# Kernel tuning notes

Hardware: AMD Instinct MI355X
Metric: run time of the kernel (lower is better)

## Reference

```python
import jax, jax.numpy as jnp
import numpy as np

B, C, T, K = 16, 256, 2048, 1024

def setup_inputs() -> dict:
    key = jax.random.key(0)
    k1, k2 = jax.random.split(key)
    z = jax.random.normal(k1, (B, C, T), dtype=jnp.float32)
    codebook = jax.random.normal(k2, (K, C), dtype=jnp.float32)
    return {"z": z, "codebook": codebook}

def reference(z, codebook):
    # z: (B, C, T) -> z_flat: (B*T, C)
    Bsz, Ch, Tlen = z.shape
    z_flat = jnp.transpose(z, (0, 2, 1)).reshape(-1, Ch)
    # squared L2 distances: |z|^2 - 2 z.c + |c|^2  -> (B*T, K)
    distances = (
        jnp.sum(z_flat * z_flat, axis=1, keepdims=True)
        - 2.0 * (z_flat @ codebook.T)
        + jnp.sum(codebook * codebook, axis=1)[None, :]
    )
    indices = jnp.argmin(distances, axis=1)            # (B*T,)
    z_q_flat = codebook[indices]                       # (B*T, C)
    z_q = jnp.transpose(z_q_flat.reshape(Bsz, Tlen, Ch), (0, 2, 1))  # (B, C, T)
    indices_reshaped = indices.reshape(Bsz, Tlen)      # (B, T)
    return z_q, indices_reshaped
```

## Files before the change

### kernel.cpp

```cpp
#include <hip/hip_runtime.h>

#define NB 16
#define NC 256
#define NT 2048
#define NK 1024
#define TQB 128
#define NCHUNKS 32
#define HALF_B 16384
#define CHUNK_B 32768
#define AMB_TH 0.05f

typedef __attribute__((ext_vector_type(8))) short short8v;
typedef __attribute__((ext_vector_type(16))) float f32x16;

__device__ __forceinline__ unsigned bf16_rne(float x) {
  unsigned u = __float_as_uint(x);
  return (u + 0x7FFFu + ((u >> 16) & 1u)) >> 16;
}

__global__ __launch_bounds__(256) void vq_prep(const float* __restrict__ cb,
                                               char* __restrict__ cbs,
                                               float* __restrict__ cnorm) {
  const int k = blockIdx.x, c = threadIdx.x;
  float v = cb[k * NC + c];
  unsigned hb = bf16_rne(v);
  float hf = __uint_as_float(hb << 16);
  unsigned lb = bf16_rne(v - hf);
  const int chunk = k >> 5, r = k & 31;
  const int off = (r << 9) + (((((c >> 3)) ^ r) & 31) << 4) + ((c & 7) << 1);
  *(unsigned short*)(cbs + (size_t)chunk * CHUNK_B + off) = (unsigned short)hb;
  *(unsigned short*)(cbs + (size_t)chunk * CHUNK_B + HALF_B + off) = (unsigned short)lb;
  float s = v * v;
  #pragma unroll
  for (int o = 32; o > 0; o >>= 1) s += __shfl_down(s, o, 64);
  __shared__ float wsum[4];
  if ((threadIdx.x & 63) == 0) wsum[threadIdx.x >> 6] = s;
  __syncthreads();
  if (threadIdx.x == 0) cnorm[k] = 0.5f * (wsum[0] + wsum[1] + wsum[2] + wsum[3]);
}

__global__ __launch_bounds__(256, 1) void vq_main(const float* __restrict__ z,
                                                  const char* __restrict__ cbs,
                                                  const float* __restrict__ cnorm,
                                                  const float* __restrict__ cb,
                                                  float* __restrict__ out,
                                                  int* __restrict__ flags) {
  __shared__ char ldsb[2 * CHUNK_B];
  __shared__ int idx_sh[TQB];
  __shared__ int amb_sh[TQB];
  const int tid = threadIdx.x;
  const int w = tid >> 6, l = tid & 63;
  const int r = l & 31;
  const int h = l >> 5;
  const int b = blockIdx.x >> 4;
  const int t0 = (blockIdx.x & 15) * TQB;
  const int tq = t0 + (w << 5) + r;

  short8v Ahi[16], Alo[16];
  #pragma unroll
  for (int s = 0; s < 16; ++s) {
    const float* zp = z + ((size_t)(b * NC + (s << 4) + (h << 3))) * NT + tq;
    #pragma unroll
    for (int e = 0; e < 8; ++e) {
      float v = zp[(size_t)e * NT];
      unsigned hb = bf16_rne(v);
      float hf = __uint_as_float(hb << 16);
      unsigned lb = bf16_rne(v - hf);
      Ahi[s][e] = (short)hb;
      Alo[s][e] = (short)lb;
    }
  }

  float bestv[16], secv[16];
  int besti[16];
  #pragma unroll
  for (int i = 0; i < 16; ++i) {
    bestv[i] = -3.402823466e38f; secv[i] = -3.402823466e38f; besti[i] = 0;
  }

#define STAGE(CH, BSEL) do {                                                      \
    const char* _s = cbs + (size_t)(CH) * CHUNK_B + ((size_t)tid << 4);           \
    char* _d = ldsb + (BSEL) * CHUNK_B + (w << 10);                               \
    _Pragma("unroll")                                                             \
    for (int _j = 0; _j < 8; ++_j)                                                \
      __builtin_amdgcn_global_load_lds(                                           \
          (const __attribute__((address_space(1))) void*)(_s + (_j << 12)),       \
          (__attribute__((address_space(3))) void*)(_d + (_j << 12)), 16, 0, 0);  \
  } while (0)

  STAGE(0, 0);
  int bufsel = 0;
  for (int ch = 0; ch < NCHUNKS; ++ch) {
    STAGE((ch + 1) & (NCHUNKS - 1), bufsel ^ 1);
    asm volatile("s_waitcnt vmcnt(8)" ::: "memory");
    __builtin_amdgcn_s_barrier();
    float cn = cnorm[(ch << 5) + r];
    f32x16 accA = {}, accB = {}, accC = {};
    const char* Lh = ldsb + bufsel * CHUNK_B;
    #pragma unroll
    for (int s = 0; s < 16; ++s) {
      const int off = (r << 9) + (((((s << 1) + h) ^ r) & 31) << 4);
      short8v Bh = *(const short8v*)(Lh + off);
      short8v Bl = *(const short8v*)(Lh + HALF_B + off);
      accA = __builtin_amdgcn_mfma_f32_32x32x16_bf16(Ahi[s], Bh, accA, 0, 0, 0);
      accB = __builtin_amdgcn_mfma_f32_32x32x16_bf16(Ahi[s], Bl, accB, 0, 0, 0);
      accC = __builtin_amdgcn_mfma_f32_32x32x16_bf16(Alo[s], Bh, accC, 0, 0, 0);
    }
    __builtin_amdgcn_s_barrier();
    const int kidx = (ch << 5) + r;
    #pragma unroll
    for (int i = 0; i < 16; ++i) {
      float sc = (accA[i] + accB[i] + accC[i]) - cn;
      if (sc > bestv[i]) { secv[i] = bestv[i]; bestv[i] = sc; besti[i] = kidx; }
      else               { secv[i] = fmaxf(secv[i], sc); }
    }
    bufsel ^= 1;
  }
#undef STAGE

  #pragma unroll
  for (int st = 1; st < 32; st <<= 1) {
    #pragma unroll
    for (int i = 0; i < 16; ++i) {
      float ob = __shfl_xor(bestv[i], st, 64);
      float os = __shfl_xor(secv[i], st, 64);
      int   oi = __shfl_xor(besti[i], st, 64);
      if (ob > bestv[i]) {
        secv[i] = fmaxf(bestv[i], os);
        bestv[i] = ob; besti[i] = oi;
      } else {
        secv[i] = fmaxf(secv[i], ob);
        if (ob == bestv[i] && oi < besti[i]) besti[i] = oi;
      }
    }
  }
  if (r == 0) {
    #pragma unroll
    for (int i = 0; i < 16; ++i) {
      const int row = (i & 3) + ((i >> 2) << 3) + (h << 2);
      idx_sh[(w << 5) + row] = besti[i];
      amb_sh[(w << 5) + row] = (bestv[i] - secv[i] <= AMB_TH) ? 1 : 0;
    }
  }
  asm volatile("s_waitcnt vmcnt(0)" ::: "memory");
  __syncthreads();

  if (tid < TQB) {
    const int t = t0 + tid;
    out[(size_t)NB * NC * NT + (size_t)b * NT + t] = (float)idx_sh[tid];
    flags[b * NT + t] = amb_sh[tid];
  }

  const int tt = tid & 127;
  const int chi = tid >> 7;
  const int myidx = idx_sh[tt];
  const float* crow = cb + (size_t)myidx * NC;
  const size_t obase = (size_t)b * NC * NT + (size_t)t0 + tt;
  #pragma unroll 8
  for (int c0 = 0; c0 < NC; c0 += 2) {
    const int c = c0 + chi;
    out[obase + (size_t)c * NT] = crow[c];
  }
}

__global__ __launch_bounds__(256) void vq_cleanup(const float* __restrict__ z,
                                                  const float* __restrict__ cb,
                                                  const int* __restrict__ flags,
                                                  float* __restrict__ out) {
  const int q = blockIdx.x;
  if (!flags[q]) return;
  const int b = q >> 11, t = q & (NT - 1);
  __shared__ float zsh[NC];
  __shared__ unsigned long long red[5];
  const int tid = threadIdx.x;
  zsh[tid] = z[((size_t)b * NC + tid) * NT + t];
  __syncthreads();
  float bd = 3.402823466e38f; int bi = NK;
  #pragma unroll
  for (int j = 0; j < 4; ++j) {
    const int k = (j << 8) + tid;
    const float* ck = cb + (size_t)k * NC;
    float d0 = 0.f, d1 = 0.f, d2 = 0.f, d3 = 0.f;
    for (int c = 0; c < NC; c += 4) {
      float4 zz = *(const float4*)&zsh[c];
      float4 cc = *(const float4*)&ck[c];
      float e0 = zz.x - cc.x, e1 = zz.y - cc.y, e2 = zz.z - cc.z, e3 = zz.w - cc.w;
      d0 = fmaf(e0, e0, d0); d1 = fmaf(e1, e1, d1);
      d2 = fmaf(e2, e2, d2); d3 = fmaf(e3, e3, d3);
    }
    float d = (d0 + d1) + (d2 + d3);
    if (d < bd) { bd = d; bi = k; }
  }
  unsigned long long p = ((unsigned long long)__float_as_uint(bd) << 32) | (unsigned)bi;
  #pragma unroll
  for (int st = 1; st < 64; st <<= 1) {
    unsigned long long o = __shfl_xor(p, st, 64);
    if (o < p) p = o;
  }
  if ((tid & 63) == 0) red[tid >> 6] = p;
  __syncthreads();
  if (tid == 0) {
    unsigned long long m = red[0];
    for (int ww = 1; ww < 4; ++ww) if (red[ww] < m) m = red[ww];
    red[4] = m;
  }
  __syncthreads();
  const int best = (int)(red[4] & 0xFFFFFFFFull);
  if (tid == 0) out[(size_t)NB * NC * NT + (size_t)b * NT + t] = (float)best;
  out[((size_t)b * NC + tid) * NT + t] = cb[(size_t)best * NC + tid];
}

extern "C" void kernel_launch(void* const* d_in, const int* in_sizes, int n_in,
                              void* d_out, int out_size, void* d_ws, size_t ws_size,
                              hipStream_t stream) {
  const float* z = (const float*)d_in[0];
  const float* cb = (const float*)d_in[1];
  float* out = (float*)d_out;
  char* cbs = (char*)d_ws;
  float* cnorm = (float*)((char*)d_ws + (size_t)NCHUNKS * CHUNK_B);
  int* flags = (int*)((char*)d_ws + (size_t)NCHUNKS * CHUNK_B + 4096);

  vq_prep<<<NK, NC, 0, stream>>>(cb, cbs, cnorm);
  vq_main<<<256, 256, 0, stream>>>(z, cbs, cnorm, cb, out, flags);
  vq_cleanup<<<NB * NT, 256, 0, stream>>>(z, cb, flags, out);
}
```

Before: 316.8 us.

## Split codebook across two blocks per tile, merge partials, compact cleanup worklist

The main kernel now launches 512 blocks, each scanning half of the codebook (16 chunks) for a 128-query tile. Each block writes partial best, second-best and index values, and a new merge kernel combines the two halves and gathers the output rows. The goal is to fill more CUs than the previous 256 blocks, and occupancy is raised to 2 blocks per CU. The ambiguity cleanup reads an atomically built worklist instead of launching one block per query, and two MFMA accumulators are merged into one to save registers. The cost is an extra kernel launch plus round-trips of the partial results through global memory.

After: 574.2 us. +81.3%, slower.

```diff
diff --git a/kernel.cpp b/kernel.cpp
--- a/kernel.cpp
+++ b/kernel.cpp
@@ -4,8 +4,8 @@
 #define NC 256
 #define NT 2048
 #define NK 1024
+#define NQ (NB * NT)
 #define TQB 128
-#define NCHUNKS 32
 #define HALF_B 16384
 #define CHUNK_B 32768
 #define AMB_TH 0.05f
@@ -20,7 +20,9 @@
 
 __global__ __launch_bounds__(256) void vq_prep(const float* __restrict__ cb,
                                                char* __restrict__ cbs,
-                                               float* __restrict__ cnorm) {
+                                               float* __restrict__ cnorm,
+                                               int* __restrict__ cnt) {
+  if (blockIdx.x == 0 && threadIdx.x == 0) *cnt = 0;
   const int k = blockIdx.x, c = threadIdx.x;
   float v = cb[k * NC + c];
   unsigned hb = bf16_rne(v);
@@ -39,21 +41,21 @@
   if (threadIdx.x == 0) cnorm[k] = 0.5f * (wsum[0] + wsum[1] + wsum[2] + wsum[3]);
 }
 
-__global__ __launch_bounds__(256, 1) void vq_main(const float* __restrict__ z,
+__global__ __launch_bounds__(256, 2) void vq_main(const float* __restrict__ z,
                                                   const char* __restrict__ cbs,
                                                   const float* __restrict__ cnorm,
-                                                  const float* __restrict__ cb,
-                                                  float* __restrict__ out,
-                                                  int* __restrict__ flags) {
+                                                  float* __restrict__ pb,
+                                                  float* __restrict__ ps,
+                                                  int* __restrict__ pi) {
   __shared__ char ldsb[2 * CHUNK_B];
-  __shared__ int idx_sh[TQB];
-  __shared__ int amb_sh[TQB];
   const int tid = threadIdx.x;
   const int w = tid >> 6, l = tid & 63;
   const int r = l & 31;
   const int h = l >> 5;
-  const int b = blockIdx.x >> 4;
-  const int t0 = (blockIdx.x & 15) * TQB;
+  const int kh = blockIdx.x >> 8;
+  const int qt = blockIdx.x & 255;
+  const int b = qt >> 4;
+  const int t0 = (qt & 15) * TQB;
   const int tq = t0 + (w << 5) + r;
 
   short8v Ahi[16], Alo[16];
@@ -88,29 +90,31 @@
           (__attribute__((address_space(3))) void*)(_d + (_j << 12)), 16, 0, 0);  \
   } while (0)
 
-  STAGE(0, 0);
+  const int ch0 = kh << 4;
+  STAGE(ch0, 0);
   int bufsel = 0;
-  for (int ch = 0; ch < NCHUNKS; ++ch) {
-    STAGE((ch + 1) & (NCHUNKS - 1), bufsel ^ 1);
+  for (int cc = 0; cc < 16; ++cc) {
+    const int ch = ch0 + cc;
+    STAGE(ch0 + ((cc + 1) & 15), bufsel ^ 1);
     asm volatile("s_waitcnt vmcnt(8)" ::: "memory");
     __builtin_amdgcn_s_barrier();
     float cn = cnorm[(ch << 5) + r];
-    f32x16 accA = {}, accB = {}, accC = {};
+    f32x16 accA = {}, accBC = {};
     const char* Lh = ldsb + bufsel * CHUNK_B;
     #pragma unroll
     for (int s = 0; s < 16; ++s) {
       const int off = (r << 9) + (((((s << 1) + h) ^ r) & 31) << 4);
       short8v Bh = *(const short8v*)(Lh + off);
       short8v Bl = *(const short8v*)(Lh + HALF_B + off);
-      accA = __builtin_amdgcn_mfma_f32_32x32x16_bf16(Ahi[s], Bh, accA, 0, 0, 0);
-      accB = __builtin_amdgcn_mfma_f32_32x32x16_bf16(Ahi[s], Bl, accB, 0, 0, 0);
-      accC = __builtin_amdgcn_mfma_f32_32x32x16_bf16(Alo[s], Bh, accC, 0, 0, 0);
+      accA  = __builtin_amdgcn_mfma_f32_32x32x16_bf16(Ahi[s], Bh, accA, 0, 0, 0);
+      accBC = __builtin_amdgcn_mfma_f32_32x32x16_bf16(Alo[s], Bh, accBC, 0, 0, 0);
+      accBC = __builtin_amdgcn_mfma_f32_32x32x16_bf16(Ahi[s], Bl, accBC, 0, 0, 0);
     }
     __builtin_amdgcn_s_barrier();
     const int kidx = (ch << 5) + r;
     #pragma unroll
     for (int i = 0; i < 16; ++i) {
-      float sc = (accA[i] + accB[i] + accC[i]) - cn;
+      float sc = (accA[i] + accBC[i]) - cn;
       if (sc > bestv[i]) { secv[i] = bestv[i]; bestv[i] = sc; besti[i] = kidx; }
       else               { secv[i] = fmaxf(secv[i], sc); }
     }
@@ -138,19 +142,37 @@
     #pragma unroll
     for (int i = 0; i < 16; ++i) {
       const int row = (i & 3) + ((i >> 2) << 3) + (h << 2);
-      idx_sh[(w << 5) + row] = besti[i];
-      amb_sh[(w << 5) + row] = (bestv[i] - secv[i] <= AMB_TH) ? 1 : 0;
+      const int qg = b * NT + t0 + (w << 5) + row;
+      const int o = kh * NQ + qg;
+      pb[o] = bestv[i]; ps[o] = secv[i]; pi[o] = besti[i];
     }
   }
   asm volatile("s_waitcnt vmcnt(0)" ::: "memory");
+}
+
+__global__ __launch_bounds__(256) void vq_merge(const float* __restrict__ cb,
+                                                const float* __restrict__ pb,
+                                                const float* __restrict__ ps,
+                                                const int* __restrict__ pi,
+                                                float* __restrict__ out,
+                                                int* __restrict__ wl,
+                                                int* __restrict__ cnt) {
+  __shared__ int idx_sh[TQB];
+  const int tid = threadIdx.x;
+  const int b = blockIdx.x >> 4;
+  const int t0 = (blockIdx.x & 15) * TQB;
+  if (tid < TQB) {
+    const int qg = b * NT + t0 + tid;
+    float b0 = pb[qg], s0 = ps[qg];           int i0 = pi[qg];
+    float b1 = pb[NQ + qg], s1 = ps[NQ + qg]; int i1 = pi[NQ + qg];
+    float bb, ss; int ii;
+    if (b0 >= b1) { bb = b0; ii = i0; ss = fmaxf(s0, b1); }
+    else          { bb = b1; ii = i1; ss = fmaxf(s1, b0); }
+    idx_sh[tid] = ii;
+    out[(size_t)NB * NC * NT + qg] = (float)ii;
+    if (bb - ss <= AMB_TH) { int p = atomicAdd(cnt, 1); wl[p] = qg; }
+  }
   __syncthreads();
-
-  if (tid < TQB) {
-    const int t = t0 + tid;
-    out[(size_t)NB * NC * NT + (size_t)b * NT + t] = (float)idx_sh[tid];
-    flags[b * NT + t] = amb_sh[tid];
-  }
-
   const int tt = tid & 127;
   const int chi = tid >> 7;
   const int myidx = idx_sh[tt];
@@ -165,49 +187,53 @@
 
 __global__ __launch_bounds__(256) void vq_cleanup(const float* __restrict__ z,
                                                   const float* __restrict__ cb,
-                                                  const int* __restrict__ flags,
+                                                  const int* __restrict__ wl,
+                                                  const int* __restrict__ cnt,
                                                   float* __restrict__ out) {
-  const int q = blockIdx.x;
-  if (!flags[q]) return;
-  const int b = q >> 11, t = q & (NT - 1);
   __shared__ float zsh[NC];
   __shared__ unsigned long long red[5];
   const int tid = threadIdx.x;
-  zsh[tid] = z[((size_t)b * NC + tid) * NT + t];
-  __syncthreads();
-  float bd = 3.402823466e38f; int bi = NK;
-  #pragma unroll
-  for (int j = 0; j < 4; ++j) {
-    const int k = (j << 8) + tid;
-    const float* ck = cb + (size_t)k * NC;
-    float d0 = 0.f, d1 = 0.f, d2 = 0.f, d3 = 0.f;
-    for (int c = 0; c < NC; c += 4) {
-      float4 zz = *(const float4*)&zsh[c];
-      float4 cc = *(const float4*)&ck[c];
-      float e0 = zz.x - cc.x, e1 = zz.y - cc.y, e2 = zz.z - cc.z, e3 = zz.w - cc.w;
-      d0 = fmaf(e0, e0, d0); d1 = fmaf(e1, e1, d1);
-      d2 = fmaf(e2, e2, d2); d3 = fmaf(e3, e3, d3);
-    }
-    float d = (d0 + d1) + (d2 + d3);
-    if (d < bd) { bd = d; bi = k; }
-  }
-  unsigned long long p = ((unsigned long long)__float_as_uint(bd) << 32) | (unsigned)bi;
-  #pragma unroll
-  for (int st = 1; st < 64; st <<= 1) {
-    unsigned long long o = __shfl_xor(p, st, 64);
-    if (o < p) p = o;
-  }
-  if ((tid & 63) == 0) red[tid >> 6] = p;
-  __syncthreads();
-  if (tid == 0) {
-    unsigned long long m = red[0];
-    for (int ww = 1; ww < 4; ++ww) if (red[ww] < m) m = red[ww];
-    red[4] = m;
-  }
-  __syncthreads();
-  const int best = (int)(red[4] & 0xFFFFFFFFull);
-  if (tid == 0) out[(size_t)NB * NC * NT + (size_t)b * NT + t] = (float)best;
-  out[((size_t)b * NC + tid) * NT + t] = cb[(size_t)best * NC + tid];
+  const int n = *cnt;
+  for (int i = blockIdx.x; i < n; i += 512) {
+    const int q = wl[i];
+    const int b = q >> 11, t = q & (NT - 1);
+    zsh[tid] = z[((size_t)b * NC + tid) * NT + t];
+    __syncthreads();
+    float bd = 3.402823466e38f; int bi = NK;
+    #pragma unroll
+    for (int j = 0; j < 4; ++j) {
+      const int k = (j << 8) + tid;
+      const float* ck = cb + (size_t)k * NC;
+      float d0 = 0.f, d1 = 0.f, d2 = 0.f, d3 = 0.f;
+      for (int c = 0; c < NC; c += 4) {
+        float4 zz = *(const float4*)&zsh[c];
+        float4 cc = *(const float4*)&ck[c];
+        float e0 = zz.x - cc.x, e1 = zz.y - cc.y, e2 = zz.z - cc.z, e3 = zz.w - cc.w;
+        d0 = fmaf(e0, e0, d0); d1 = fmaf(e1, e1, d1);
+        d2 = fmaf(e2, e2, d2); d3 = fmaf(e3, e3, d3);
+      }
+      float d = (d0 + d1) + (d2 + d3);
+      if (d < bd) { bd = d; bi = k; }
+    }
+    unsigned long long p = ((unsigned long long)__float_as_uint(bd) << 32) | (unsigned)bi;
+    #pragma unroll
+    for (int st = 1; st < 64; st <<= 1) {
+      unsigned long long o = __shfl_xor(p, st, 64);
+      if (o < p) p = o;
+    }
+    if ((tid & 63) == 0) red[tid >> 6] = p;
+    __syncthreads();
+    if (tid == 0) {
+      unsigned long long m = red[0];
+      for (int ww = 1; ww < 4; ++ww) if (red[ww] < m) m = red[ww];
+      red[4] = m;
+    }
+    __syncthreads();
+    const int best = (int)(red[4] & 0xFFFFFFFFull);
+    if (tid == 0) out[(size_t)NB * NC * NT + q] = (float)best;
+    out[((size_t)b * NC + tid) * NT + t] = cb[(size_t)best * NC + tid];
+    __syncthreads();
+  }
 }
 
 extern "C" void kernel_launch(void* const* d_in, const int* in_sizes, int n_in,
@@ -216,11 +242,17 @@
   const float* z = (const float*)d_in[0];
   const float* cb = (const float*)d_in[1];
   float* out = (float*)d_out;
-  char* cbs = (char*)d_ws;
-  float* cnorm = (float*)((char*)d_ws + (size_t)NCHUNKS * CHUNK_B);
-  int* flags = (int*)((char*)d_ws + (size_t)NCHUNKS * CHUNK_B + 4096);
-
-  vq_prep<<<NK, NC, 0, stream>>>(cb, cbs, cnorm);
-  vq_main<<<256, 256, 0, stream>>>(z, cbs, cnorm, cb, out, flags);
-  vq_cleanup<<<NB * NT, 256, 0, stream>>>(z, cb, flags, out);
-}
+  char* base = (char*)d_ws;
+  char* cbs    = base;
+  float* cnorm = (float*)(base + (1 << 20));
+  int* cnt     = (int*)(base + (1 << 20) + 4096);
+  int* wl      = (int*)(base + (1 << 20) + 8192);
+  float* pb    = (float*)(base + (1 << 20) + 8192 + (128 << 10));
+  float* ps    = pb + 2 * NQ;
+  int*   pi    = (int*)(ps + 2 * NQ);
+
+  vq_prep<<<NK, NC, 0, stream>>>(cb, cbs, cnorm, cnt);
+  vq_main<<<512, 256, 0, stream>>>(z, cbs, cnorm, pb, ps, pi);
+  vq_merge<<<256, 256, 0, stream>>>(cb, pb, ps, pi, out, wl, cnt);
+  vq_cleanup<<<512, 256, 0, stream>>>(z, cb, wl, cnt, out);
+}
```
